# Kernel optimization log

Hardware: AMD Instinct MI355X
Metric: run time of the kernel (lower is better)

## Reference

```python
import jax, jax.numpy as jnp
import numpy as np

N_QUBITS = 4
EMBED_DIM = 768
FFN_DIM = 3072


def setup_inputs() -> dict:
    key = jax.random.key(0)
    ks = jax.random.split(key, 6)
    B, T = 8, 2048
    x = jax.random.normal(ks[0], (B, T, EMBED_DIM), dtype=jnp.float32)
    # trainable RY angles (torchquantum RY has_params=True init)
    theta = jax.random.uniform(ks[1], (N_QUBITS,), dtype=jnp.float32, minval=-np.pi, maxval=np.pi)
    # linear1: n_qubits -> ffn_dim ; linear2: ffn_dim -> embed_dim
    W1 = jax.random.normal(ks[2], (N_QUBITS, FFN_DIM), dtype=jnp.float32) / np.sqrt(N_QUBITS)
    b1 = jnp.zeros((FFN_DIM,), dtype=jnp.float32)
    W2 = jax.random.normal(ks[3], (FFN_DIM, EMBED_DIM), dtype=jnp.float32) / np.sqrt(FFN_DIM)
    b2 = jnp.zeros((EMBED_DIM,), dtype=jnp.float32)
    return {"x": x, "theta": theta, "W1": W1, "b1": b1, "W2": W2, "b2": b2}


def reference(x, theta, W1, b1, W2, b2):
    # x: [B, T, C]; take first n_qubits features as RX encoder angles (C > n_qubits)
    ang = x[..., :N_QUBITS]  # [B, T, Q]
    # Circuit per sample: |0> -RX(ang_i)-> -RY(theta_i)-> measure PauliZ on wire i.
    # All gates are single-qubit (product state); exact expectation:
    #   RX(a)|0> has Bloch vector (0, -sin a, cos a); RY(t) rotates about y:
    #   <Z> = cos(a) * cos(t).  Same math as the sequential state-vector sim, fused.
    q_out = jnp.cos(ang) * jnp.cos(theta)  # [B, T, Q]
    # dropout is identity in eval mode
    h = jax.nn.relu(jnp.einsum('btq,qf->btf', q_out, W1) + b1)  # [B, T, F]
    out = jnp.einsum('btf,fe->bte', h, W2) + b2                  # [B, T, E]
    return out
```

## Files before the change

kernel.cpp:

```cpp
#include <hip/hip_runtime.h>
#include <hip/hip_bf16.h>
#include <math.h>
#include <stdint.h>


typedef __bf16 bf16_t;
typedef __attribute__((ext_vector_type(8))) __bf16 bf16x8;
typedef __attribute__((ext_vector_type(4))) float f32x4;

#define M_TOT 16384
#define E_DIM 768
#define F_DIM 3072

constexpr int BM = 128, BN = 128, BK = 64;
constexpr int MT = M_TOT / BM;
constexpr int NT = E_DIM / BN;
constexpr int KT = F_DIM / BK;
constexpr int KT2 = 2 * KT;
constexpr int BTILE = 12288;
constexpr int NT4 = 4;

constexpr size_t WS_B2   = 0;
constexpr size_t WS_G    = WS_B2 + (size_t)NT4 * KT2 * BTILE;
constexpr size_t WS_NEED = WS_G + (size_t)M_TOT * 16;

__global__ __launch_bounds__(256)
void ffq_prep(const float* __restrict__ x, const float* __restrict__ theta,
              const float* __restrict__ W2, char* __restrict__ ws)
{
    const int t = threadIdx.x;
    const int bid = blockIdx.x;

    if (bid < 64) {
        const int m = bid * 256 + t;
        const float4 xv = *reinterpret_cast<const float4*>(x + (size_t)m * E_DIM);
        float4 g;
        g.x = cosf(xv.x) * cosf(theta[0]);
        g.y = cosf(xv.y) * cosf(theta[1]);
        g.z = cosf(xv.z) * cosf(theta[2]);
        g.w = cosf(xv.w) * cosf(theta[3]);
        *reinterpret_cast<float4*>(ws + WS_G + (size_t)m * 16) = g;
    } else {
        __shared__ float Wf[64][196];
        const int idx = bid - 64;
        const int kt  = idx >> 2;
        const int nt  = idx & 3;
        #pragma unroll
        for (int ii = 0; ii < 12; ++ii) {
            const int q = ii * 256 + t;
            const int row = q / 48;
            const int c4  = (q % 48) * 4;
            const float4 v = *reinterpret_cast<const float4*>(
                &W2[(size_t)(kt * 64 + row) * E_DIM + nt * 192 + c4]);
            Wf[row][c4] = v.x; Wf[row][c4 + 1] = v.y;
            Wf[row][c4 + 2] = v.z; Wf[row][c4 + 3] = v.w;
        }
        __syncthreads();
        char* base = ws + WS_B2 + (size_t)(nt * KT2 + 2 * kt) * BTILE;
        #pragma unroll
        for (int cc = 0; cc < 6; ++cc) {
            const int c    = cc * 256 + t;
            const int half = c / 768;
            const int q    = c - half * 768;
            const int rb   = q >> 2;
            const int slot = q & 3;
            const int oc   = slot ^ ((rb >> 1) & 3);
            bf16x8 v;
            #pragma unroll
            for (int j = 0; j < 8; ++j) v[j] = (bf16_t)Wf[half * 32 + oc * 8 + j][rb];
            *reinterpret_cast<bf16x8*>(base + (size_t)half * BTILE + (size_t)q * 16) = v;
        }
    }
}

__global__ __launch_bounds__(512, 1)
void ffq_gemm(const char* __restrict__ ws, const float* __restrict__ W1,
              const float* __restrict__ b1, const float* __restrict__ b2,
              float* __restrict__ out)
{
    __shared__ float4 W1sm[F_DIM];
    __shared__ float  b1sm[F_DIM];

    const int t = threadIdx.x;
    const int lane = t & 63, wid = t >> 6;

    const int bid = blockIdx.x;
    const int xcd = bid & 7;
    const int i   = bid >> 3;
    const int mtb = xcd * 8 + (i & 7);
    const int nt  = i >> 3;
    const int m0 = mtb * 256, n0 = nt * 192;

    const int wrm = wid & 3;
    const int wcn = wid >> 2;
    const int fr = lane & 15, fg = lane >> 4;

    const char* srcB = ws + WS_B2 + (size_t)nt * KT2 * BTILE;
    const float4* garr = reinterpret_cast<const float4*>(ws + WS_G);

    #pragma unroll
    for (int ii = 0; ii < 6; ++ii) {
        const int k = ii * 512 + t;
        W1sm[k] = make_float4(W1[k], W1[F_DIM + k], W1[2 * F_DIM + k],
                              W1[3 * F_DIM + k]);
        b1sm[k] = b1[k];
    }

    float4 g4[4];
    #pragma unroll
    for (int mi = 0; mi < 4; ++mi)
        g4[mi] = garr[m0 + wrm * 64 + mi * 16 + fr];

    __syncthreads();

    int offB[6];
    #pragma unroll
    for (int ni = 0; ni < 6; ++ni) {
        const int rb = wcn * 96 + ni * 16 + fr;
        const int sl = fg ^ ((rb >> 1) & 3);
        offB[ni] = rb * 64 + sl * 16;
    }

    f32x4 acc[4][6] = {};
    bf16x8 fa0[4], fa1[4], fb0[6], fb1[6];

    #define AGEN(kk, FA) do {                                                   \
        const int kb_ = (kk) * 32 + fg * 8;                                     \
        _Pragma("unroll")                                                       \
        for (int hh = 0; hh < 2; ++hh) {                                        \
            float4 w_[4];                                                       \
            _Pragma("unroll")                                                   \
            for (int j = 0; j < 4; ++j) w_[j] = W1sm[kb_ + hh * 4 + j];         \
            const float4 bv_ = *reinterpret_cast<const float4*>(&b1sm[kb_ + hh * 4]); \
            const float b_[4] = {bv_.x, bv_.y, bv_.z, bv_.w};                   \
            _Pragma("unroll")                                                   \
            for (int mi = 0; mi < 4; ++mi) {                                    \
                _Pragma("unroll")                                               \
                for (int j = 0; j < 4; ++j) {                                   \
                    float p_ = b_[j];                                           \
                    p_ = fmaf(g4[mi].x, w_[j].x, p_);                           \
                    p_ = fmaf(g4[mi].y, w_[j].y, p_);                           \
                    p_ = fmaf(g4[mi].z, w_[j].z, p_);                           \
                    p_ = fmaf(g4[mi].w, w_[j].w, p_);                           \
                    FA[mi][hh * 4 + j] = (bf16_t)fmaxf(p_, 0.0f);               \
                }                                                               \
            }                                                                   \
        } } while (0)

    #define LOADB(kk, FB) do {                                                  \
        const char* sb_ = srcB + (size_t)(kk) * BTILE;                          \
        _Pragma("unroll")                                                       \
        for (int ni = 0; ni < 6; ++ni)                                          \
            FB[ni] = *reinterpret_cast<const bf16x8*>(sb_ + offB[ni]);          \
        } while (0)

    #define MFMA24(FA, FB) do {                                                 \
        _Pragma("unroll")                                                       \
        for (int mi = 0; mi < 4; ++mi)                                          \
            _Pragma("unroll")                                                   \
            for (int ni = 0; ni < 6; ++ni)                                      \
                acc[mi][ni] = __builtin_amdgcn_mfma_f32_16x16x32_bf16(          \
                    FA[mi], FB[ni], acc[mi][ni], 0, 0, 0);                      \
        } while (0)

    LOADB(0, fb0); AGEN(0, fa0);
    LOADB(1, fb1); AGEN(1, fa1);

    for (int p = 0; p < KT2 / 2 - 1; ++p) {
        MFMA24(fa0, fb0);
        LOADB(2 * p + 2, fb0);
        AGEN(2 * p + 2, fa0);
        MFMA24(fa1, fb1);
        LOADB(2 * p + 3, fb1);
        AGEN(2 * p + 3, fa1);
    }
    MFMA24(fa0, fb0);
    MFMA24(fa1, fb1);

    #undef AGEN
    #undef LOADB
    #undef MFMA24

    #pragma unroll
    for (int ni = 0; ni < 6; ++ni) {
        const int col = n0 + wcn * 96 + ni * 16 + fr;
        const float bias = b2[col];
        #pragma unroll
        for (int mi = 0; mi < 4; ++mi) {
            #pragma unroll
            for (int rr = 0; rr < 4; ++rr) {
                const int ro = m0 + wrm * 64 + mi * 16 + fg * 4 + rr;
                out[(size_t)ro * E_DIM + col] = acc[mi][ni][rr] + bias;
            }
        }
    }
}

__global__ __launch_bounds__(256, 2)
void ffq_fused(const float* __restrict__ x, const float* __restrict__ theta,
               const float* __restrict__ W1, const float* __restrict__ b1,
               const float* __restrict__ W2, const float* __restrict__ b2,
               float* __restrict__ out)
{
    __shared__ bf16_t Asm[BM][BK];
    __shared__ bf16_t Bsm[BN][BK];
    __shared__ float  gsm[BM][4];
    __shared__ float  b2sm[BN];

    const int t = threadIdx.x;
    const int lane = t & 63, wid = t >> 6;
    const int bid = blockIdx.x;
    const int swz = (bid & 7) * (MT * NT / 8) + (bid >> 3);
    const int ntile = swz / MT, mtile = swz % MT;
    const int m0 = mtile * BM, n0 = ntile * BN;

    const float c0 = cosf(theta[0]), c1 = cosf(theta[1]);
    const float c2 = cosf(theta[2]), c3 = cosf(theta[3]);
    if (t < BM) {
        const float4 xv = *reinterpret_cast<const float4*>(x + (size_t)(m0 + t) * E_DIM);
        gsm[t][0] = cosf(xv.x) * c0; gsm[t][1] = cosf(xv.y) * c1;
        gsm[t][2] = cosf(xv.z) * c2; gsm[t][3] = cosf(xv.w) * c3;
    } else {
        const int n = t - 128;
        b2sm[n] = b2[n0 + n];
    }
    __syncthreads();

    const int rg = t >> 3, kg = t & 7;
    const int nB = t & 127, kh = t >> 7;
    const int wr = wid >> 1, wc = wid & 1;
    const int fr = lane & 15, fg = lane >> 4;

    f32x4 acc[4][4] = {};

    for (int k0 = 0; k0 < F_DIM; k0 += BK) {
        {
            const int kA = k0 + (kg << 3);
            float w1v[4][8], b1v[8];
            #pragma unroll
            for (int q = 0; q < 4; ++q) {
                const float4 lo = *reinterpret_cast<const float4*>(&W1[q * F_DIM + kA]);
                const float4 hi = *reinterpret_cast<const float4*>(&W1[q * F_DIM + kA + 4]);
                w1v[q][0] = lo.x; w1v[q][1] = lo.y; w1v[q][2] = lo.z; w1v[q][3] = lo.w;
                w1v[q][4] = hi.x; w1v[q][5] = hi.y; w1v[q][6] = hi.z; w1v[q][7] = hi.w;
            }
            {
                const float4 lo = *reinterpret_cast<const float4*>(&b1[kA]);
                const float4 hi = *reinterpret_cast<const float4*>(&b1[kA + 4]);
                b1v[0] = lo.x; b1v[1] = lo.y; b1v[2] = lo.z; b1v[3] = lo.w;
                b1v[4] = hi.x; b1v[5] = hi.y; b1v[6] = hi.z; b1v[7] = hi.w;
            }
            #pragma unroll
            for (int r = 0; r < 4; ++r) {
                const int row = (rg << 2) + r;
                const float4 g = *reinterpret_cast<const float4*>(&gsm[row][0]);
                bf16x8 v;
                #pragma unroll
                for (int kk = 0; kk < 8; ++kk) {
                    float p = b1v[kk];
                    p = fmaf(g.x, w1v[0][kk], p);
                    p = fmaf(g.y, w1v[1][kk], p);
                    p = fmaf(g.z, w1v[2][kk], p);
                    p = fmaf(g.w, w1v[3][kk], p);
                    v[kk] = (bf16_t)fmaxf(p, 0.0f);
                }
                *reinterpret_cast<bf16x8*>(&Asm[row][(kg ^ (row & 7)) << 3]) = v;
            }
        }
        {
            const float* w2p = W2 + (size_t)(k0 + (kh << 5)) * E_DIM + n0 + nB;
            float bv[32];
            #pragma unroll
            for (int kk = 0; kk < 32; ++kk) bv[kk] = w2p[kk * E_DIM];
            #pragma unroll
            for (int o = 0; o < 4; ++o) {
                bf16x8 v;
                #pragma unroll
                for (int j = 0; j < 8; ++j) v[j] = (bf16_t)bv[(o << 3) + j];
                *reinterpret_cast<bf16x8*>(&Bsm[nB][(((kh << 2) + o) ^ (nB & 7)) << 3]) = v;
            }
        }
        __syncthreads();
        #pragma unroll
        for (int ks = 0; ks < 2; ++ks) {
            const int kob = (ks << 2) + fg;
            bf16x8 af[4], bfr[4];
            #pragma unroll
            for (int mi = 0; mi < 4; ++mi) {
                const int row = (wr << 6) + (mi << 4) + fr;
                af[mi] = *reinterpret_cast<const bf16x8*>(&Asm[row][(kob ^ (row & 7)) << 3]);
            }
            #pragma unroll
            for (int ni = 0; ni < 4; ++ni) {
                const int rn = (wc << 6) + (ni << 4) + fr;
                bfr[ni] = *reinterpret_cast<const bf16x8*>(&Bsm[rn][(kob ^ (rn & 7)) << 3]);
            }
            #pragma unroll
            for (int mi = 0; mi < 4; ++mi)
                #pragma unroll
                for (int ni = 0; ni < 4; ++ni)
                    acc[mi][ni] = __builtin_amdgcn_mfma_f32_16x16x32_bf16(
                        af[mi], bfr[ni], acc[mi][ni], 0, 0, 0);
        }
        __syncthreads();
    }

    #pragma unroll
    for (int mi = 0; mi < 4; ++mi)
        #pragma unroll
        for (int ni = 0; ni < 4; ++ni) {
            const int col  = n0 + (wc << 6) + (ni << 4) + fr;
            const float bias = b2sm[(wc << 6) + (ni << 4) + fr];
            #pragma unroll
            for (int r = 0; r < 4; ++r) {
                const int row = m0 + (wr << 6) + (mi << 4) + (fg << 2) + r;
                out[(size_t)row * E_DIM + col] = acc[mi][ni][r] + bias;
            }
        }
}

extern "C" void kernel_launch(void* const* d_in, const int* in_sizes, int n_in,
                              void* d_out, int out_size, void* d_ws, size_t ws_size,
                              hipStream_t stream) {
    const float* x     = (const float*)d_in[0];
    const float* theta = (const float*)d_in[1];
    const float* W1    = (const float*)d_in[2];
    const float* b1    = (const float*)d_in[3];
    const float* W2    = (const float*)d_in[4];
    const float* b2    = (const float*)d_in[5];
    float* out = (float*)d_out;

    if (ws_size >= WS_NEED) {
        hipLaunchKernelGGL(ffq_prep, dim3(256), dim3(256), 0, stream,
                           x, theta, W2, (char*)d_ws);
        hipLaunchKernelGGL(ffq_gemm, dim3(256), dim3(512), 0, stream,
                           (const char*)d_ws, W1, b1, b2, out);
    } else {
        hipLaunchKernelGGL(ffq_fused, dim3(MT * NT), dim3(256), 0, stream,
                           x, theta, W1, b1, W2, b2, out);
    }
}
```

Before: 103.6 us.

## Compute hidden activations with packed fp16 math and switch MFMA to f16

```diff
diff --git a/kernel.cpp b/kernel.cpp
--- a/kernel.cpp
+++ b/kernel.cpp
@@ -6,7 +6,11 @@
 
 typedef __bf16 bf16_t;
 typedef __attribute__((ext_vector_type(8))) __bf16 bf16x8;
+typedef __attribute__((ext_vector_type(8))) _Float16 f16x8;
+typedef __attribute__((ext_vector_type(2))) _Float16 f16x2;
 typedef __attribute__((ext_vector_type(4))) float f32x4;
+
+struct F16x2x4 { f16x2 v[4]; };
 
 #define M_TOT 16384
 #define E_DIM 768
@@ -65,10 +69,10 @@
             const int rb   = q >> 2;
             const int slot = q & 3;
             const int oc   = slot ^ ((rb >> 1) & 3);
-            bf16x8 v;
-            #pragma unroll
-            for (int j = 0; j < 8; ++j) v[j] = (bf16_t)Wf[half * 32 + oc * 8 + j][rb];
-            *reinterpret_cast<bf16x8*>(base + (size_t)half * BTILE + (size_t)q * 16) = v;
+            f16x8 v;
+            #pragma unroll
+            for (int j = 0; j < 8; ++j) v[j] = (_Float16)Wf[half * 32 + oc * 8 + j][rb];
+            *reinterpret_cast<f16x8*>(base + (size_t)half * BTILE + (size_t)q * 16) = v;
         }
     }
 }
@@ -78,8 +82,8 @@
               const float* __restrict__ b1, const float* __restrict__ b2,
               float* __restrict__ out)
 {
-    __shared__ float4 W1sm[F_DIM];
-    __shared__ float  b1sm[F_DIM];
+    __shared__ __align__(16) f16x2 W1i[F_DIM / 2][4];
+    __shared__ f16x2 b1h[F_DIM / 2];
 
     const int t = threadIdx.x;
     const int lane = t & 63, wid = t >> 6;
@@ -99,17 +103,33 @@
     const float4* garr = reinterpret_cast<const float4*>(ws + WS_G);
 
     #pragma unroll
-    for (int ii = 0; ii < 6; ++ii) {
-        const int k = ii * 512 + t;
-        W1sm[k] = make_float4(W1[k], W1[F_DIM + k], W1[2 * F_DIM + k],
-                              W1[3 * F_DIM + k]);
-        b1sm[k] = b1[k];
+    for (int ii = 0; ii < 3; ++ii) {
+        const int kp = ii * 512 + t;
+        #pragma unroll
+        for (int q = 0; q < 4; ++q) {
+            const float2 a = *reinterpret_cast<const float2*>(&W1[(size_t)q * F_DIM + 2 * kp]);
+            f16x2 w; w[0] = (_Float16)a.x; w[1] = (_Float16)a.y;
+            W1i[kp][q] = w;
+        }
+        const float2 bb = *reinterpret_cast<const float2*>(&b1[2 * kp]);
+        f16x2 bh; bh[0] = (_Float16)bb.x; bh[1] = (_Float16)bb.y;
+        b1h[kp] = bh;
     }
 
     float4 g4[4];
     #pragma unroll
     for (int mi = 0; mi < 4; ++mi)
         g4[mi] = garr[m0 + wrm * 64 + mi * 16 + fr];
+
+    f16x2 gx2[4], gy2[4], gz2[4], gw2[4];
+    #pragma unroll
+    for (int mi = 0; mi < 4; ++mi) {
+        gx2[mi][0] = (_Float16)g4[mi].x; gx2[mi][1] = (_Float16)g4[mi].x;
+        gy2[mi][0] = (_Float16)g4[mi].y; gy2[mi][1] = (_Float16)g4[mi].y;
+        gz2[mi][0] = (_Float16)g4[mi].z; gz2[mi][1] = (_Float16)g4[mi].z;
+        gw2[mi][0] = (_Float16)g4[mi].w; gw2[mi][1] = (_Float16)g4[mi].w;
+    }
+    const f16x2 zero2 = {(_Float16)0.0f, (_Float16)0.0f};
 
     __syncthreads();
 
@@ -122,36 +142,38 @@
     }
 
     f32x4 acc[4][6] = {};
-    bf16x8 fa0[4], fa1[4], fb0[6], fb1[6];
+    f16x8 fa0[4], fa1[4], fb0[6], fb1[6];
 
     #define AGEN(kk, FA) do {                                                   \
-        const int kb_ = (kk) * 32 + fg * 8;                                     \
+        const int kp0_ = (kk) * 16 + fg * 4;                                    \
+        f16x2 pm_[4][4];                                                        \
         _Pragma("unroll")                                                       \
-        for (int hh = 0; hh < 2; ++hh) {                                        \
-            float4 w_[4];                                                       \
-            _Pragma("unroll")                                                   \
-            for (int j = 0; j < 4; ++j) w_[j] = W1sm[kb_ + hh * 4 + j];         \
-            const float4 bv_ = *reinterpret_cast<const float4*>(&b1sm[kb_ + hh * 4]); \
-            const float b_[4] = {bv_.x, bv_.y, bv_.z, bv_.w};                   \
+        for (int c_ = 0; c_ < 4; ++c_) {                                        \
+            const F16x2x4 wr_ = *reinterpret_cast<const F16x2x4*>(&W1i[kp0_ + c_][0]); \
+            const f16x2 bp_ = b1h[kp0_ + c_];                                   \
             _Pragma("unroll")                                                   \
             for (int mi = 0; mi < 4; ++mi) {                                    \
-                _Pragma("unroll")                                               \
-                for (int j = 0; j < 4; ++j) {                                   \
-                    float p_ = b_[j];                                           \
-                    p_ = fmaf(g4[mi].x, w_[j].x, p_);                           \
-                    p_ = fmaf(g4[mi].y, w_[j].y, p_);                           \
-                    p_ = fmaf(g4[mi].z, w_[j].z, p_);                           \
-                    p_ = fmaf(g4[mi].w, w_[j].w, p_);                           \
-                    FA[mi][hh * 4 + j] = (bf16_t)fmaxf(p_, 0.0f);               \
-                }                                                               \
+                f16x2 p_ = bp_;                                                 \
+                p_ = __builtin_elementwise_fma(gx2[mi], wr_.v[0], p_);          \
+                p_ = __builtin_elementwise_fma(gy2[mi], wr_.v[1], p_);          \
+                p_ = __builtin_elementwise_fma(gz2[mi], wr_.v[2], p_);          \
+                p_ = __builtin_elementwise_fma(gw2[mi], wr_.v[3], p_);          \
+                pm_[mi][c_] = __builtin_elementwise_max(p_, zero2);             \
             }                                                                   \
+        }                                                                       \
+        _Pragma("unroll")                                                       \
+        for (int mi = 0; mi < 4; ++mi) {                                        \
+            F16x2x4 t_;                                                         \
+            t_.v[0] = pm_[mi][0]; t_.v[1] = pm_[mi][1];                         \
+            t_.v[2] = pm_[mi][2]; t_.v[3] = pm_[mi][3];                         \
+            FA[mi] = __builtin_bit_cast(f16x8, t_);                             \
         } } while (0)
 
     #define LOADB(kk, FB) do {                                                  \
         const char* sb_ = srcB + (size_t)(kk) * BTILE;                          \
         _Pragma("unroll")                                                       \
         for (int ni = 0; ni < 6; ++ni)                                          \
-            FB[ni] = *reinterpret_cast<const bf16x8*>(sb_ + offB[ni]);          \
+            FB[ni] = *reinterpret_cast<const f16x8*>(sb_ + offB[ni]);           \
         } while (0)
 
     #define MFMA24(FA, FB) do {                                                 \
@@ -159,7 +181,7 @@
         for (int mi = 0; mi < 4; ++mi)                                          \
             _Pragma("unroll")                                                   \
             for (int ni = 0; ni < 6; ++ni)                                      \
-                acc[mi][ni] = __builtin_amdgcn_mfma_f32_16x16x32_bf16(          \
+                acc[mi][ni] = __builtin_amdgcn_mfma_f32_16x16x32_f16(           \
                     FA[mi], FB[ni], acc[mi][ni], 0, 0, 0);                      \
         } while (0)
 
```

After: 84.34 us. -18.6%, faster.
